# Kernel tuning notes

Hardware: AMD Instinct MI355X
Metric: run time of the kernel (lower is better)

Reference implementation:

```python
import jax, jax.numpy as jnp
import numpy as np

NUM_GRAPHS = 256
BN_EPS = 1e-5


def _bn(x, g, b, m, v):
    # eval-mode BatchNorm1d: affine with running stats
    return (x - m) * jax.lax.rsqrt(v + BN_EPS) * g + b


def setup_inputs() -> dict:
    key = jax.random.key(0)
    ks = jax.random.split(key, 16)
    N = 500_000
    x = jax.random.normal(ks[0], (N, 3), dtype=jnp.float32)
    batch = jnp.sort(jax.random.randint(ks[1], (N,), 0, NUM_GRAPHS, dtype=jnp.int32))

    def lin(k, fan_in, fan_out):
        kw, kb = jax.random.split(k)
        s = 1.0 / np.sqrt(fan_in)
        W = jax.random.uniform(kw, (fan_in, fan_out), jnp.float32, -s, s)
        b = jax.random.uniform(kb, (fan_out,), jnp.float32, -s, s)
        return W, b

    def bn_params(k, dim):
        k1, k2, k3, k4 = jax.random.split(k, 4)
        g = 1.0 + 0.05 * jax.random.normal(k1, (dim,), jnp.float32)
        be = 0.05 * jax.random.normal(k2, (dim,), jnp.float32)
        m = 0.05 * jax.random.normal(k3, (dim,), jnp.float32)
        v = 0.5 + jax.random.uniform(k4, (dim,), jnp.float32)
        return g, be, m, v

    W1, b1 = lin(ks[2], 3, 64)
    g1, be1, m1, v1 = bn_params(ks[3], 64)
    W2, b2 = lin(ks[4], 64, 64)          # plain last layer of local MLP
    W3, b3 = lin(ks[5], 64, 128)
    g3, be3, m3, v3 = bn_params(ks[6], 128)
    W4, b4 = lin(ks[7], 128, 1024)       # plain last layer of global MLP

    return {
        "x": x, "batch": batch,
        "W1": W1, "b1": b1, "g1": g1, "be1": be1, "m1": m1, "v1": v1,
        "W2": W2, "b2": b2,
        "W3": W3, "b3": b3, "g3": g3, "be3": be3, "m3": m3, "v3": v3,
        "W4": W4, "b4": b4,
    }


def reference(x, batch, W1, b1, g1, be1, m1, v1, W2, b2,
              W3, b3, g3, be3, m3, v3, W4, b4):
    # local MLP [3, 64, 64]: Linear->BN->ReLU, plain last
    h = jax.nn.relu(_bn(x @ W1 + b1, g1, be1, m1, v1))   # [N, 64]
    h = h @ W2 + b2                                       # [N, 64]
    # global MLP [64, 128, 1024]: Linear->BN->ReLU, plain last
    h = jax.nn.relu(_bn(h @ W3 + b3, g3, be3, m3, v3))    # [N, 128]
    h = h @ W4 + b4                                       # [N, 1024]
    # global_max_pool: ragged scatter-max over per-point graph ids
    out = jax.ops.segment_max(h, batch, num_segments=NUM_GRAPHS)  # [G, 1024]
    return out
```

## Files before the change

### kernel.cpp

```cpp
#include <hip/hip_runtime.h>
#include <hip/hip_bf16.h>
#include <cstdint>

typedef __attribute__((ext_vector_type(8))) short bf16x8;
typedef __attribute__((ext_vector_type(4))) float f32x4;

#define BN_EPS 1e-5f

__device__ __forceinline__ unsigned short f2bf(float f) {
    unsigned int u = __float_as_uint(f);
    unsigned int r = (u + 0x7FFFu + ((u >> 16) & 1u)) >> 16;
    return (unsigned short)r;
}
__device__ __forceinline__ float bf2f(unsigned short h) {
    return __uint_as_float(((unsigned int)h) << 16);
}
__device__ __forceinline__ unsigned int encf(float f) {
    unsigned int u = __float_as_uint(f);
    return (u & 0x80000000u) ? ~u : (u | 0x80000000u);
}

__device__ __forceinline__ long long lbound(const int* __restrict__ b, long long n, int key) {
    long long lo = 0, hi = n;
    while (lo < hi) { long long mid = (lo + hi) >> 1; if (b[mid] < key) lo = mid + 1; else hi = mid; }
    return lo;
}

__global__ void fold_kernel(const float* __restrict__ W1, const float* __restrict__ b1,
                            const float* __restrict__ g1, const float* __restrict__ be1,
                            const float* __restrict__ m1, const float* __restrict__ v1,
                            const float* __restrict__ W2, const float* __restrict__ b2,
                            const float* __restrict__ W3, const float* __restrict__ b3,
                            const float* __restrict__ g3, const float* __restrict__ be3,
                            const float* __restrict__ m3, const float* __restrict__ v3,
                            const float* __restrict__ W4,
                            unsigned short* __restrict__ W4p,
                            unsigned short* __restrict__ W23ph, unsigned short* __restrict__ W23pl,
                            float* __restrict__ W1c, float* __restrict__ b23) {
    int tid = blockIdx.x * blockDim.x + threadIdx.x;
    if (tid < 131072) {
        int j = tid & 7, lane = (tid >> 3) & 63, kf = (tid >> 9) & 3, nt = tid >> 11;
        int col = nt * 16 + (lane & 15);
        int k = kf * 32 + (lane >> 4) * 8 + j;
        W4p[tid] = f2bf(W4[k * 1024 + col]);
    }
    if (tid < 8192) {
        int j = tid & 7, lane = (tid >> 3) & 63, kf = (tid >> 9) & 1, nn = tid >> 10;
        int col = nn * 16 + (lane & 15);
        int k = kf * 32 + (lane >> 4) * 8 + j;
        float s3 = g3[col] / sqrtf(v3[col] + BN_EPS);
        float acc = 0.f;
        for (int o = 0; o < 64; ++o) acc += W2[k * 64 + o] * W3[o * 128 + col];
        float w = acc * s3;
        unsigned short hi = f2bf(w);
        W23ph[tid] = hi;
        W23pl[tid] = f2bf(w - bf2f(hi));
    }
    if (tid < 128) {
        float s3 = g3[tid] / sqrtf(v3[tid] + BN_EPS);
        float acc = b3[tid] - m3[tid];
        for (int o = 0; o < 64; ++o) acc += b2[o] * W3[o * 128 + tid];
        b23[tid] = acc * s3 + be3[tid];
    }
    if (tid < 256) {
        int o = tid >> 2, c = tid & 3;
        float s1 = g1[o] / sqrtf(v1[o] + BN_EPS);
        W1c[tid] = (c < 3) ? W1[c * 64 + o] * s1 : (b1[o] - m1[o]) * s1 + be1[o];
    }
}

__global__ __launch_bounds__(64) void fused_kernel(const float* __restrict__ x,
                                                   const float* __restrict__ W1c,
                                                   const unsigned short* __restrict__ W23ph,
                                                   const unsigned short* __restrict__ W23pl,
                                                   const float* __restrict__ b23,
                                                   const unsigned short* __restrict__ W4p,
                                                   const float* __restrict__ b4,
                                                   const int* __restrict__ batch,
                                                   unsigned int* __restrict__ out,
                                                   float* __restrict__ tilemax,
                                                   int* __restrict__ gtile,
                                                   long long pbase, int ntiles, long long Ntot) {
    __shared__ unsigned short h3[64 * 136];
    int wave = blockIdx.x;
    if (wave >= ntiles) return;
    int lane = threadIdx.x & 63;
    int q = lane >> 4, r16 = lane & 15;
    long long p0 = pbase + (long long)wave * 64;

    float xv[4][3];
    bool valid[4];
#pragma unroll
    for (int mt = 0; mt < 4; ++mt) {
        long long p = p0 + mt * 16 + r16;
        if (p < Ntot) {
            xv[mt][0] = x[p * 3 + 0]; xv[mt][1] = x[p * 3 + 1]; xv[mt][2] = x[p * 3 + 2];
            valid[mt] = true;
        } else {
            xv[mt][0] = xv[mt][1] = xv[mt][2] = 0.f; valid[mt] = false;
        }
    }
    bf16x8 a2[4][2];
#pragma unroll
    for (int kf = 0; kf < 2; ++kf)
#pragma unroll
        for (int j = 0; j < 8; ++j) {
            int f = kf * 32 + q * 8 + j;
            float4 w = *reinterpret_cast<const float4*>(W1c + f * 4);
#pragma unroll
            for (int mt = 0; mt < 4; ++mt) {
                float v = fmaf(xv[mt][0], w.x, fmaf(xv[mt][1], w.y, fmaf(xv[mt][2], w.z, w.w)));
                v = valid[mt] ? fmaxf(v, 0.f) : 0.f;
                a2[mt][kf][j] = (short)f2bf(v);
            }
        }

#pragma unroll
    for (int half = 0; half < 2; ++half) {
        f32x4 acc2[4][4];
#pragma unroll
        for (int mt = 0; mt < 4; ++mt)
#pragma unroll
            for (int n = 0; n < 4; ++n) acc2[mt][n] = (f32x4){0.f, 0.f, 0.f, 0.f};
#pragma unroll
        for (int n = 0; n < 4; ++n) {
            int nn = half * 4 + n;
#pragma unroll
            for (int kf = 0; kf < 2; ++kf) {
                bf16x8 bh = *reinterpret_cast<const bf16x8*>(W23ph + (size_t)((nn * 2 + kf) * 64 + lane) * 8);
                bf16x8 bl = *reinterpret_cast<const bf16x8*>(W23pl + (size_t)((nn * 2 + kf) * 64 + lane) * 8);
#pragma unroll
                for (int mt = 0; mt < 4; ++mt) {
                    acc2[mt][n] = __builtin_amdgcn_mfma_f32_16x16x32_bf16(a2[mt][kf], bh, acc2[mt][n], 0, 0, 0);
                    acc2[mt][n] = __builtin_amdgcn_mfma_f32_16x16x32_bf16(a2[mt][kf], bl, acc2[mt][n], 0, 0, 0);
                }
            }
        }
#pragma unroll
        for (int n = 0; n < 4; ++n) {
            int col = (half * 4 + n) * 16 + r16;
            float bias = b23[col];
#pragma unroll
            for (int mt = 0; mt < 4; ++mt)
#pragma unroll
                for (int r = 0; r < 4; ++r) {
                    int row = mt * 16 + q * 4 + r;
                    float v = fmaxf(acc2[mt][n][r] + bias, 0.f);
                    h3[row * 136 + col] = f2bf(v);
                }
        }
    }
    asm volatile("s_waitcnt lgkmcnt(0)" ::: "memory");

    bf16x8 a[4][4];
#pragma unroll
    for (int mt = 0; mt < 4; ++mt)
#pragma unroll
        for (int kf = 0; kf < 4; ++kf)
            a[mt][kf] = *reinterpret_cast<const bf16x8*>(h3 + (16 * mt + r16) * 136 + kf * 32 + q * 8);

    long long plast = p0 + 63; if (plast > Ntot - 1) plast = Ntot - 1;
    int gfirst = batch[(p0 < Ntot) ? p0 : (Ntot - 1)];
    int glast = batch[plast];
    bool fast = (gfirst == glast) && (p0 + 63 < Ntot);
    if (lane == 0) gtile[wave] = fast ? gfirst : -1;

    if (fast) {
        float* tm = tilemax + (size_t)wave * 1024;
        const unsigned short* wp = W4p + (size_t)lane * 8;
        for (int g8 = 0; g8 < 8; ++g8) {
            float m8[8];
#pragma unroll
            for (int pr = 0; pr < 4; ++pr) {
                const unsigned short* w0 = wp + (size_t)(g8 * 8 + pr * 2) * 2048;
                bf16x8 b0[4], b1[4];
#pragma unroll
                for (int kf = 0; kf < 4; ++kf) {
                    b0[kf] = *reinterpret_cast<const bf16x8*>(w0 + kf * 512);
                    b1[kf] = *reinterpret_cast<const bf16x8*>(w0 + 2048 + kf * 512);
                }
                f32x4 aA[4], aB[4];
#pragma unroll
                for (int m = 0; m < 4; ++m) { aA[m] = (f32x4){0.f,0.f,0.f,0.f}; aB[m] = (f32x4){0.f,0.f,0.f,0.f}; }
#pragma unroll
                for (int kf = 0; kf < 4; ++kf)
#pragma unroll
                    for (int m = 0; m < 4; ++m) {
                        aA[m] = __builtin_amdgcn_mfma_f32_16x16x32_bf16(a[m][kf], b0[kf], aA[m], 0, 0, 0);
                        aB[m] = __builtin_amdgcn_mfma_f32_16x16x32_bf16(a[m][kf], b1[kf], aB[m], 0, 0, 0);
                    }
                float mA = fmaxf(fmaxf(fmaxf(aA[0][0], aA[0][1]), fmaxf(aA[0][2], aA[0][3])),
                                 fmaxf(fmaxf(aA[1][0], aA[1][1]), fmaxf(aA[1][2], aA[1][3])));
                mA = fmaxf(mA, fmaxf(fmaxf(fmaxf(aA[2][0], aA[2][1]), fmaxf(aA[2][2], aA[2][3])),
                                     fmaxf(fmaxf(aA[3][0], aA[3][1]), fmaxf(aA[3][2], aA[3][3]))));
                float mB = fmaxf(fmaxf(fmaxf(aB[0][0], aB[0][1]), fmaxf(aB[0][2], aB[0][3])),
                                 fmaxf(fmaxf(aB[1][0], aB[1][1]), fmaxf(aB[1][2], aB[1][3])));
                mB = fmaxf(mB, fmaxf(fmaxf(fmaxf(aB[2][0], aB[2][1]), fmaxf(aB[2][2], aB[2][3])),
                                     fmaxf(fmaxf(aB[3][0], aB[3][1]), fmaxf(aB[3][2], aB[3][3]))));
                m8[pr * 2] = mA; m8[pr * 2 + 1] = mB;
            }
#pragma unroll
            for (int qq = 0; qq < 8; ++qq) {
                float v = m8[qq];
                v = fmaxf(v, __shfl_xor(v, 16));
                v = fmaxf(v, __shfl_xor(v, 32));
                m8[qq] = v;
            }
            if (lane < 16) {
#pragma unroll
                for (int qq = 0; qq < 8; ++qq) tm[(g8 * 8 + qq) * 16 + lane] = m8[qq];
            }
        }
        return;
    }

    int gl = -1;
    unsigned long long smask = 0;
    int grow[16];
    {
        long long pl = p0 + lane;
        gl = (pl < Ntot) ? batch[pl] : -1;
        int gprev = __shfl_up(gl, 1);
        bool is_start = (lane == 0) || (gl != gprev);
        smask = __ballot(is_start);
#pragma unroll
        for (int m = 0; m < 4; ++m)
#pragma unroll
            for (int r = 0; r < 4; ++r) {
                int rw = m * 16 + (lane >> 4) * 4 + r;
                grow[m * 4 + r] = __shfl(gl, rw);
            }
    }

    for (int nt = 0; nt < 64; ++nt) {
        bf16x8 bq[4];
#pragma unroll
        for (int kf = 0; kf < 4; ++kf)
            bq[kf] = *reinterpret_cast<const bf16x8*>(W4p + (size_t)((nt * 4 + kf) * 64 + lane) * 8);
        f32x4 acc[4];
#pragma unroll
        for (int m = 0; m < 4; ++m) acc[m] = (f32x4){0.f, 0.f, 0.f, 0.f};
#pragma unroll
        for (int kf = 0; kf < 4; ++kf)
#pragma unroll
            for (int m = 0; m < 4; ++m)
                acc[m] = __builtin_amdgcn_mfma_f32_16x16x32_bf16(a[m][kf], bq[kf], acc[m], 0, 0, 0);

        int col = nt * 16 + (lane & 15);
        float bias = b4[col];
        unsigned long long tmp = smask;
        while (tmp) {
            int ls = __builtin_ctzll(tmp); tmp &= tmp - 1;
            int gs = __shfl(gl, ls);
            float m = -INFINITY;
#pragma unroll
            for (int mm = 0; mm < 4; ++mm)
#pragma unroll
                for (int r = 0; r < 4; ++r)
                    if (grow[mm * 4 + r] == gs) m = fmaxf(m, acc[mm][r]);
            m = fmaxf(m, __shfl_xor(m, 16));
            m = fmaxf(m, __shfl_xor(m, 32));
            if (gs >= 0 && lane < 16 && m > -INFINITY)
                atomicMax(&out[gs * 1024 + col], encf(m + bias));
        }
    }
}

__global__ __launch_bounds__(256) void reduce_chunk(const float* __restrict__ tilemax,
                                                    const int* __restrict__ gtile,
                                                    const int* __restrict__ batch,
                                                    const float* __restrict__ b4,
                                                    unsigned int* __restrict__ out,
                                                    long long base, long long npts, long long N) {
    int g = blockIdx.x >> 2;
    int col = (blockIdx.x & 3) * 256 + threadIdx.x;
    __shared__ int sh[2];
    if (threadIdx.x == 0) {
        long long lo = lbound(batch, N, g);
        long long hi = lbound(batch, N, g + 1);
        long long e = base + npts;
        if (lo < base) lo = base;
        if (hi > e) hi = e;
        sh[0] = (int)(lo - base);
        sh[1] = (int)(hi - base);
    }
    __syncthreads();
    int lo = sh[0], hi = sh[1];
    if (lo >= hi) return;
    int t0 = lo >> 6, t1 = (hi - 1) >> 6;
    float m = -INFINITY;
    for (int t = t0; t <= t1; ++t)
        if (gtile[t] == g) m = fmaxf(m, tilemax[(size_t)t * 1024 + col]);
    if (m > -INFINITY) atomicMax(&out[g * 1024 + col], encf(m + b4[col]));
}

__global__ void init_out(unsigned int* out, int n) {
    int t = blockIdx.x * 256 + threadIdx.x;
    if (t < n) out[t] = 0x007FFFFFu;
}
__global__ void decode_out(unsigned int* out, int n) {
    int t = blockIdx.x * 256 + threadIdx.x;
    if (t < n) {
        unsigned int e = out[t];
        out[t] = (e & 0x80000000u) ? (e & 0x7FFFFFFFu) : ~e;
    }
}

extern "C" void kernel_launch(void* const* d_in, const int* in_sizes, int n_in,
                              void* d_out, int out_size, void* d_ws, size_t ws_size,
                              hipStream_t stream) {
    const float* x   = (const float*)d_in[0];
    const int* batch = (const int*)d_in[1];
    const float* W1  = (const float*)d_in[2];
    const float* b1  = (const float*)d_in[3];
    const float* g1  = (const float*)d_in[4];
    const float* be1 = (const float*)d_in[5];
    const float* m1  = (const float*)d_in[6];
    const float* v1  = (const float*)d_in[7];
    const float* W2  = (const float*)d_in[8];
    const float* b2  = (const float*)d_in[9];
    const float* W3  = (const float*)d_in[10];
    const float* b3  = (const float*)d_in[11];
    const float* g3  = (const float*)d_in[12];
    const float* be3 = (const float*)d_in[13];
    const float* m3  = (const float*)d_in[14];
    const float* v3  = (const float*)d_in[15];
    const float* W4  = (const float*)d_in[16];
    const float* b4  = (const float*)d_in[17];

    long long N = in_sizes[1];

    char* ws = (char*)d_ws;
    unsigned short* W4p   = (unsigned short*)(ws + 0);
    unsigned short* W23ph = (unsigned short*)(ws + 262144);
    unsigned short* W23pl = (unsigned short*)(ws + 278528);
    float* W1c = (float*)(ws + 294912);
    float* b23 = (float*)(ws + 295936);

    fold_kernel<<<512, 256, 0, stream>>>(W1, b1, g1, be1, m1, v1, W2, b2, W3, b3, g3, be3, m3, v3,
                                         W4, W4p, W23ph, W23pl, W1c, b23);
    init_out<<<(out_size + 255) / 256, 256, 0, stream>>>((unsigned int*)d_out, out_size);

    const size_t ofs = 1 << 20;
    size_t avail = (ws_size > ofs) ? ws_size - ofs : 0;
    long long Tcap = (long long)(avail / 4104);
    Tcap &= ~3LL;
    if (Tcap < 4) Tcap = 4;
    long long ntiles_tot = (N + 63) / 64;
    long long ntcap = (ntiles_tot + 3) & ~3LL;
    if (Tcap > ntcap) Tcap = ntcap;

    float* tilemax = (float*)(ws + ofs);
    int* gtile = (int*)(ws + ofs + (size_t)Tcap * 4096);
    long long chunk = Tcap * 64;

    for (long long base = 0; base < N; base += chunk) {
        long long npts = N - base; if (npts > chunk) npts = chunk;
        int ntiles = (int)((npts + 63) / 64);
        fused_kernel<<<ntiles, 64, 0, stream>>>(x, W1c, W23ph, W23pl, b23, W4p, b4, batch,
                                                (unsigned int*)d_out, tilemax, gtile,
                                                base, ntiles, N);
        reduce_chunk<<<1024, 256, 0, stream>>>(tilemax, gtile, batch, b4, (unsigned int*)d_out,
                                               base, npts, N);
    }
    decode_out<<<(out_size + 255) / 256, 256, 0, stream>>>((unsigned int*)d_out, out_size);
}
```

Measured before the change: 244.0 us.

## Cut register and LDS use to raise occupancy, double-buffer W4 fragment loads

Requests four waves per SIMD via launch bounds and shrinks the shared h3 staging buffer by processing the 128-wide hidden layer in two halves, reading A fragments after each half. The layer-4 loop now computes one 16-column tile at a time with a double-buffered prefetch of the next tile's W4 fragments, replacing the paired two-tile accumulators. The aim is to free VGPRs and LDS so more waves stay resident and global weight-load latency is hidden. It adds extra LDS wait points, and the register cap may force spills.

New measurement: 207.6 us. -14.9%, faster.

```diff
diff --git a/kernel.cpp b/kernel.cpp
--- a/kernel.cpp
+++ b/kernel.cpp
@@ -69,19 +69,19 @@
     }
 }
 
-__global__ __launch_bounds__(64) void fused_kernel(const float* __restrict__ x,
-                                                   const float* __restrict__ W1c,
-                                                   const unsigned short* __restrict__ W23ph,
-                                                   const unsigned short* __restrict__ W23pl,
-                                                   const float* __restrict__ b23,
-                                                   const unsigned short* __restrict__ W4p,
-                                                   const float* __restrict__ b4,
-                                                   const int* __restrict__ batch,
-                                                   unsigned int* __restrict__ out,
-                                                   float* __restrict__ tilemax,
-                                                   int* __restrict__ gtile,
-                                                   long long pbase, int ntiles, long long Ntot) {
-    __shared__ unsigned short h3[64 * 136];
+__global__ __launch_bounds__(64, 4) void fused_kernel(const float* __restrict__ x,
+                                                      const float* __restrict__ W1c,
+                                                      const unsigned short* __restrict__ W23ph,
+                                                      const unsigned short* __restrict__ W23pl,
+                                                      const float* __restrict__ b23,
+                                                      const unsigned short* __restrict__ W4p,
+                                                      const float* __restrict__ b4,
+                                                      const int* __restrict__ batch,
+                                                      unsigned int* __restrict__ out,
+                                                      float* __restrict__ tilemax,
+                                                      int* __restrict__ gtile,
+                                                      long long pbase, int ntiles, long long Ntot) {
+    __shared__ unsigned short h3[64 * 72];
     int wave = blockIdx.x;
     if (wave >= ntiles) return;
     int lane = threadIdx.x & 63;
@@ -115,49 +115,45 @@
             }
         }
 
+    bf16x8 a[4][4];
 #pragma unroll
     for (int half = 0; half < 2; ++half) {
-        f32x4 acc2[4][4];
-#pragma unroll
-        for (int mt = 0; mt < 4; ++mt)
-#pragma unroll
-            for (int n = 0; n < 4; ++n) acc2[mt][n] = (f32x4){0.f, 0.f, 0.f, 0.f};
 #pragma unroll
         for (int n = 0; n < 4; ++n) {
             int nn = half * 4 + n;
+            f32x4 acc2[4];
+#pragma unroll
+            for (int mt = 0; mt < 4; ++mt) acc2[mt] = (f32x4){0.f, 0.f, 0.f, 0.f};
 #pragma unroll
             for (int kf = 0; kf < 2; ++kf) {
                 bf16x8 bh = *reinterpret_cast<const bf16x8*>(W23ph + (size_t)((nn * 2 + kf) * 64 + lane) * 8);
                 bf16x8 bl = *reinterpret_cast<const bf16x8*>(W23pl + (size_t)((nn * 2 + kf) * 64 + lane) * 8);
 #pragma unroll
                 for (int mt = 0; mt < 4; ++mt) {
-                    acc2[mt][n] = __builtin_amdgcn_mfma_f32_16x16x32_bf16(a2[mt][kf], bh, acc2[mt][n], 0, 0, 0);
-                    acc2[mt][n] = __builtin_amdgcn_mfma_f32_16x16x32_bf16(a2[mt][kf], bl, acc2[mt][n], 0, 0, 0);
+                    acc2[mt] = __builtin_amdgcn_mfma_f32_16x16x32_bf16(a2[mt][kf], bh, acc2[mt], 0, 0, 0);
+                    acc2[mt] = __builtin_amdgcn_mfma_f32_16x16x32_bf16(a2[mt][kf], bl, acc2[mt], 0, 0, 0);
                 }
             }
-        }
-#pragma unroll
-        for (int n = 0; n < 4; ++n) {
-            int col = (half * 4 + n) * 16 + r16;
+            int col = nn * 16 + r16;
             float bias = b23[col];
 #pragma unroll
             for (int mt = 0; mt < 4; ++mt)
 #pragma unroll
                 for (int r = 0; r < 4; ++r) {
                     int row = mt * 16 + q * 4 + r;
-                    float v = fmaxf(acc2[mt][n][r] + bias, 0.f);
-                    h3[row * 136 + col] = f2bf(v);
+                    float v = fmaxf(acc2[mt][r] + bias, 0.f);
+                    h3[row * 72 + n * 16 + r16] = f2bf(v);
                 }
         }
-    }
-    asm volatile("s_waitcnt lgkmcnt(0)" ::: "memory");
-
-    bf16x8 a[4][4];
-#pragma unroll
-    for (int mt = 0; mt < 4; ++mt)
-#pragma unroll
-        for (int kf = 0; kf < 4; ++kf)
-            a[mt][kf] = *reinterpret_cast<const bf16x8*>(h3 + (16 * mt + r16) * 136 + kf * 32 + q * 8);
+        asm volatile("s_waitcnt lgkmcnt(0)" ::: "memory");
+#pragma unroll
+        for (int mt = 0; mt < 4; ++mt)
+#pragma unroll
+            for (int kfl = 0; kfl < 2; ++kfl)
+                a[mt][half * 2 + kfl] =
+                    *reinterpret_cast<const bf16x8*>(h3 + (16 * mt + r16) * 72 + kfl * 32 + q * 8);
+        asm volatile("s_waitcnt lgkmcnt(0)" ::: "memory");
+    }
 
     long long plast = p0 + 63; if (plast > Ntot - 1) plast = Ntot - 1;
     int gfirst = batch[(p0 < Ntot) ? p0 : (Ntot - 1)];
@@ -168,36 +164,36 @@
     if (fast) {
         float* tm = tilemax + (size_t)wave * 1024;
         const unsigned short* wp = W4p + (size_t)lane * 8;
+        bf16x8 Bp[2][4];
+#pragma unroll
+        for (int kf = 0; kf < 4; ++kf)
+            Bp[0][kf] = *reinterpret_cast<const bf16x8*>(wp + (size_t)kf * 512);
+
         for (int g8 = 0; g8 < 8; ++g8) {
             float m8[8];
 #pragma unroll
-            for (int pr = 0; pr < 4; ++pr) {
-                const unsigned short* w0 = wp + (size_t)(g8 * 8 + pr * 2) * 2048;
-                bf16x8 b0[4], b1[4];
-#pragma unroll
-                for (int kf = 0; kf < 4; ++kf) {
-                    b0[kf] = *reinterpret_cast<const bf16x8*>(w0 + kf * 512);
-                    b1[kf] = *reinterpret_cast<const bf16x8*>(w0 + 2048 + kf * 512);
+            for (int i8 = 0; i8 < 8; ++i8) {
+                int nt = g8 * 8 + i8;
+                const int cur = i8 & 1, nxt = cur ^ 1;
+                {
+                    const unsigned short* wq = wp + (size_t)(((nt + 1) & 63) * 4) * 512;
+#pragma unroll
+                    for (int kf = 0; kf < 4; ++kf)
+                        Bp[nxt][kf] = *reinterpret_cast<const bf16x8*>(wq + (size_t)kf * 512);
                 }
-                f32x4 aA[4], aB[4];
-#pragma unroll
-                for (int m = 0; m < 4; ++m) { aA[m] = (f32x4){0.f,0.f,0.f,0.f}; aB[m] = (f32x4){0.f,0.f,0.f,0.f}; }
+                f32x4 acc[4];
+#pragma unroll
+                for (int mt = 0; mt < 4; ++mt) acc[mt] = (f32x4){0.f, 0.f, 0.f, 0.f};
 #pragma unroll
                 for (int kf = 0; kf < 4; ++kf)
 #pragma unroll
-                    for (int m = 0; m < 4; ++m) {
-                        aA[m] = __builtin_amdgcn_mfma_f32_16x16x32_bf16(a[m][kf], b0[kf], aA[m], 0, 0, 0);
-                        aB[m] = __builtin_amdgcn_mfma_f32_16x16x32_bf16(a[m][kf], b1[kf], aB[m], 0, 0, 0);
-                    }
-                float mA = fmaxf(fmaxf(fmaxf(aA[0][0], aA[0][1]), fmaxf(aA[0][2], aA[0][3])),
-                                 fmaxf(fmaxf(aA[1][0], aA[1][1]), fmaxf(aA[1][2], aA[1][3])));
-                mA = fmaxf(mA, fmaxf(fmaxf(fmaxf(aA[2][0], aA[2][1]), fmaxf(aA[2][2], aA[2][3])),
-                                     fmaxf(fmaxf(aA[3][0], aA[3][1]), fmaxf(aA[3][2], aA[3][3]))));
-                float mB = fmaxf(fmaxf(fmaxf(aB[0][0], aB[0][1]), fmaxf(aB[0][2], aB[0][3])),
-                                 fmaxf(fmaxf(aB[1][0], aB[1][1]), fmaxf(aB[1][2], aB[1][3])));
-                mB = fmaxf(mB, fmaxf(fmaxf(fmaxf(aB[2][0], aB[2][1]), fmaxf(aB[2][2], aB[2][3])),
-                                     fmaxf(fmaxf(aB[3][0], aB[3][1]), fmaxf(aB[3][2], aB[3][3]))));
-                m8[pr * 2] = mA; m8[pr * 2 + 1] = mB;
+                    for (int mt = 0; mt < 4; ++mt)
+                        acc[mt] = __builtin_amdgcn_mfma_f32_16x16x32_bf16(a[mt][kf], Bp[cur][kf], acc[mt], 0, 0, 0);
+                float m = fmaxf(fmaxf(fmaxf(acc[0][0], acc[0][1]), fmaxf(acc[0][2], acc[0][3])),
+                                fmaxf(fmaxf(acc[1][0], acc[1][1]), fmaxf(acc[1][2], acc[1][3])));
+                m = fmaxf(m, fmaxf(fmaxf(fmaxf(acc[2][0], acc[2][1]), fmaxf(acc[2][2], acc[2][3])),
+                                   fmaxf(fmaxf(acc[3][0], acc[3][1]), fmaxf(acc[3][2], acc[3][3]))));
+                m8[i8] = m;
             }
 #pragma unroll
             for (int qq = 0; qq < 8; ++qq) {
```
